# Kernel tuning notes

Hardware: AMD Instinct MI355X
Metric: run time of the kernel (lower is better)

## Reference

```python
import jax, jax.numpy as jnp
import numpy as np

B, L, F = 8, 2048, 4
DM, DI, N, DCONV, DTRANK = 320, 1280, 16, 8, 20  # d_model, d_inner, d_state, d_conv, dt_rank
NBLK = 4


def setup_inputs() -> dict:
    key = jax.random.key(0)
    ks = jax.random.split(key, 24)
    s = 0.05
    inp = {
        "x": jax.random.uniform(ks[0], (B, L, F), jnp.float32),
        "fc_w": jax.random.normal(ks[1], (320, 4), jnp.float32) * s,
        "fc_b": jnp.zeros((320,), jnp.float32),
        "blk_lin_w": jax.random.normal(ks[2], (NBLK, 320, 320), jnp.float32) * s,
        "blk_lin_b": jnp.zeros((NBLK, 320), jnp.float32),
        "blk_inproj_w": jax.random.normal(ks[3], (NBLK, 2 * DI, DM), jnp.float32) * s,
        "blk_conv_w": jax.random.normal(ks[4], (NBLK, DI, DCONV), jnp.float32) * s,
        "blk_conv_b": jnp.zeros((NBLK, DI), jnp.float32),
        "blk_xproj_w": jax.random.normal(ks[5], (NBLK, DTRANK + 2 * N, DI), jnp.float32) * s,
        "blk_dtproj_w": jax.random.normal(ks[6], (NBLK, DI, DTRANK), jnp.float32) * s,
        "blk_dtproj_b": jnp.full((NBLK, DI), -4.0, jnp.float32),  # softplus(-4) ~ 0.018, stable dt
        "blk_A_log": jnp.tile(jnp.log(jnp.arange(1, N + 1, dtype=jnp.float32)), (NBLK, DI, 1)),
        "blk_D": jnp.ones((NBLK, DI), jnp.float32),
        "blk_outproj_w": jax.random.normal(ks[7], (NBLK, DM, DI), jnp.float32) * s,
        "s1_w1": jax.random.normal(ks[8], (512, 320), jnp.float32) * s,
        "s1_b1": jnp.zeros((512,), jnp.float32),
        "s1_w2": jax.random.normal(ks[9], (512, 512), jnp.float32) * s,
        "s1_b2": jnp.zeros((512,), jnp.float32),
        "s1_w3": jax.random.normal(ks[10], (1, 512), jnp.float32) * s,
        "s1_b3": jnp.zeros((1,), jnp.float32),
    }
    return inp


def _mamba(u, inproj_w, conv_w, conv_b, xproj_w, dtproj_w, dtproj_b, A_log, D):
    # u: (B, L, DM)
    xz = u @ inproj_w.T                       # (B, L, 2*DI)
    x, z = jnp.split(xz, 2, axis=-1)
    # causal depthwise conv1d over time
    xc = jnp.transpose(x, (0, 2, 1))          # (B, DI, L)
    xc = jax.lax.conv_general_dilated(
        xc, conv_w[:, None, :], (1,), [(DCONV - 1, 0)],
        feature_group_count=DI, dimension_numbers=("NCH", "OIH", "NCH"))
    xc = xc + conv_b[None, :, None]
    x = jax.nn.silu(jnp.transpose(xc, (0, 2, 1)))  # (B, L, DI)
    dbc = x @ xproj_w.T                        # (B, L, DTRANK + 2N)
    dt, Bm, Cm = jnp.split(dbc, [DTRANK, DTRANK + N], axis=-1)
    delta = jax.nn.softplus(dt @ dtproj_w.T + dtproj_b)  # (B, L, DI)
    A = -jnp.exp(A_log)                        # (DI, N)

    def step(h, inp):
        xt, dt_t, Bt, Ct = inp                 # (B,DI),(B,DI),(B,N),(B,N)
        dA = jnp.exp(dt_t[..., None] * A)      # (B, DI, N)
        h = dA * h + (dt_t * xt)[..., None] * Bt[:, None, :]
        y = jnp.einsum("bdn,bn->bd", h, Ct)
        return h, y

    h0 = jnp.zeros((u.shape[0], DI, N), x.dtype)
    xs = (jnp.swapaxes(x, 0, 1), jnp.swapaxes(delta, 0, 1),
          jnp.swapaxes(Bm, 0, 1), jnp.swapaxes(Cm, 0, 1))
    _, ys = jax.lax.scan(step, h0, xs)         # ys: (L, B, DI)
    y = jnp.swapaxes(ys, 0, 1) + x * D         # (B, L, DI)
    y = y * jax.nn.silu(z)
    return y


def reference(x, fc_w, fc_b, blk_lin_w, blk_lin_b, blk_inproj_w, blk_conv_w,
              blk_conv_b, blk_xproj_w, blk_dtproj_w, blk_dtproj_b, blk_A_log,
              blk_D, blk_outproj_w, s1_w1, s1_b1, s1_w2, s1_b2, s1_w3, s1_b3):
    seq_len = x.shape[1]
    start_max = jnp.max(x[:, :, 2])
    xn = jnp.stack([x[:, :, 0] / 255.0,
                    x[:, :, 1] / 255.0,
                    x[:, :, 2] / start_max,
                    x[:, :, 3]], axis=-1)
    out = xn @ fc_w.T + fc_b                   # (B, L, 320)
    for i in range(NBLK):
        out = jnp.tanh(out @ blk_lin_w[i].T + blk_lin_b[i])
        out = _mamba(out, blk_inproj_w[i], blk_conv_w[i], blk_conv_b[i],
                     blk_xproj_w[i], blk_dtproj_w[i], blk_dtproj_b[i],
                     blk_A_log[i], blk_D[i]) @ blk_outproj_w[i].T
        out = jax.nn.elu(out)                  # dropout p=1e-6 -> identity (eval)
    h = out[:, -1, :]                          # (B, 320)
    h = jax.nn.relu(h @ s1_w1.T + s1_b1)
    h = jax.nn.relu(h @ s1_w2.T + s1_b2)
    h = h @ s1_w3.T + s1_b3                    # (B, 1)
    scale = start_max / (1.0 + np.log(seq_len))
    h = h.at[:, 0].multiply(scale)
    return jax.nn.relu(h)
```

## Files before the change

kernel.cpp:

```cpp
#include <hip/hip_runtime.h>
#include <math.h>

#define BSZ 8
#define LSZ 2048
#define DMV 320
#define DIV 1280
#define NST 16
#define DCV 8
#define DTR 20
#define NBLKV 4
#define MTOT (BSZ*LSZ)
#define NCHUNK 32
#define CLEN 64
#define DBLD 56

typedef __attribute__((ext_vector_type(8))) short short8;
typedef __attribute__((ext_vector_type(8))) unsigned short ushort8;
typedef __attribute__((ext_vector_type(4))) float floatx4;

__device__ inline unsigned short f2bf(float f) {
    union { float f; unsigned u; } v; v.f = f;
    unsigned r = v.u + 0x7FFFu + ((v.u >> 16) & 1u);
    return (unsigned short)(r >> 16);
}
__device__ inline float bf2f(unsigned short b) {
    union { unsigned u; float f; } v; v.u = ((unsigned)b) << 16;
    return v.f;
}

__device__ __forceinline__ void gload_lds16(unsigned short* l, const unsigned short* g) {
    __builtin_amdgcn_global_load_lds(
        (const __attribute__((address_space(1))) unsigned int*)g,
        (__attribute__((address_space(3))) unsigned int*)l, 16, 0, 0);
}

__global__ __launch_bounds__(256) void convert_kernel(
    const float* __restrict__ src, unsigned short* __restrict__ dst, long n4) {
    long i = (long)blockIdx.x * 256 + threadIdx.x;
    if (i >= n4) return;
    float4 v = *(const float4*)(src + i * 4);
    unsigned short o[4] = {f2bf(v.x), f2bf(v.y), f2bf(v.z), f2bf(v.w)};
    *(unsigned long long*)(dst + i * 4) = *(unsigned long long*)o;
}

__global__ __launch_bounds__(256) void convert_dtw_kernel(
    const float* __restrict__ src, unsigned short* __restrict__ dst) {
    int i = blockIdx.x * 256 + threadIdx.x;
    if (i >= NBLKV * DIV * 32) return;
    int l = i / (DIV * 32), rem = i % (DIV * 32);
    int d = rem >> 5, j = rem & 31;
    dst[i] = (j < DTR) ? f2bf(src[((long)l * DIV + d) * DTR + j]) : (unsigned short)0;
}

__global__ __launch_bounds__(256) void convert_xp_kernel(
    const float* __restrict__ src, unsigned short* __restrict__ dst) {
    int i = blockIdx.x * 256 + threadIdx.x;
    if (i >= NBLKV * 64 * DIV) return;
    int l = i / (64 * DIV), rem = i % (64 * DIV);
    int n = rem / DIV, k = rem % DIV;
    dst[i] = (n < DTR + 2 * NST) ? f2bf(src[((long)l * (DTR + 2 * NST) + n) * DIV + k])
                                 : (unsigned short)0;
}

__global__ __launch_bounds__(256) void convert_t2_kernel(
    const float* __restrict__ src, unsigned short* __restrict__ dst, int N, int K) {
    int i = blockIdx.x * 256 + threadIdx.x;
    if (i >= N * K) return;
    int n = i / K, k = i % K;
    dst[((k >> 1) * N + n) * 2 + (k & 1)] = f2bf(src[i]);
}

__global__ void init_sm_kernel(float* sm) {
    if (threadIdx.x == 0) ((int*)sm)[0] = 0;
}

__global__ void reduce_max_kernel(const float* __restrict__ x, float* sm) {
    int idx = blockIdx.x * blockDim.x + threadIdx.x;
    float v = 0.f;
    for (int i = idx; i < MTOT; i += gridDim.x * blockDim.x)
        v = fmaxf(v, x[i * 4 + 2]);
    #pragma unroll
    for (int off = 32; off > 0; off >>= 1)
        v = fmaxf(v, __shfl_xor(v, off, 64));
    if ((threadIdx.x & 63) == 0)
        atomicMax((int*)sm, __float_as_int(v));
}

__global__ __launch_bounds__(256) void fc_kernel(
    const float* __restrict__ x, const float* __restrict__ fw,
    const float* __restrict__ fb, const float* __restrict__ sm,
    unsigned short* __restrict__ u) {
    int o = blockIdx.x * 64 + (threadIdx.x & 63);
    long m = (long)blockIdx.y * 4 + (threadIdx.x >> 6);
    float inv_sm = 1.0f / sm[0];
    float x0 = x[m * 4 + 0] * (1.0f / 255.0f);
    float x1 = x[m * 4 + 1] * (1.0f / 255.0f);
    float x2 = x[m * 4 + 2] * inv_sm;
    float x3 = x[m * 4 + 3];
    float acc = fb[o];
    acc = fmaf(x0, fw[o * 4 + 0], acc);
    acc = fmaf(x1, fw[o * 4 + 1], acc);
    acc = fmaf(x2, fw[o * 4 + 2], acc);
    acc = fmaf(x3, fw[o * 4 + 3], acc);
    u[m * DMV + o] = f2bf(acc);
}

template<int ACT, int BM, int BN, int KB, typename TOUT>
__global__ __launch_bounds__(256) void gemm_mfma_kernel(
    const unsigned short* __restrict__ X, const unsigned short* __restrict__ W,
    const float* __restrict__ bias, TOUT* __restrict__ Y,
    int N, int K, long ldx, long ldy)
{
    constexpr int WMT = (BM == 128 && BN == 128) ? 4 : 2;
    constexpr int WNT = (BM == 64 && BN == 64) ? 2 : 4;
    constexpr int CPR = KB / 8;
    constexpr int CMSK = CPR - 1;
    constexpr int NCX = BM * CPR / 256;
    constexpr int NCW = BN * CPR / 256;
    __shared__ unsigned short Xs[BM * KB];
    __shared__ unsigned short Ws[BN * KB];

    int tid = threadIdx.x;
    int wave = tid >> 6, lane = tid & 63;
    int quad = lane >> 4, l15 = lane & 15;
    int wmbase, wnbase;
    if (BM == 128 && BN == 128)      { wmbase = (wave & 1) * 64; wnbase = (wave >> 1) * 64; }
    else if (BM == 128 && BN == 64)  { wmbase = wave * 32;       wnbase = 0; }
    else                             { wmbase = (wave & 1) * 32; wnbase = (wave >> 1) * 32; }
    long m0 = (long)blockIdx.y * BM;
    int n0 = blockIdx.x * BN;

    floatx4 acc[WMT][WNT];
    #pragma unroll
    for (int i = 0; i < WMT; i++)
        #pragma unroll
        for (int j = 0; j < WNT; j++)
            acc[i][j] = (floatx4){0.f, 0.f, 0.f, 0.f};

    const unsigned short* Xb = X + m0 * ldx;
    const unsigned short* Wb = W + (long)n0 * K;

    for (int k0 = 0; k0 < K; k0 += KB) {
        #pragma unroll
        for (int j = 0; j < NCX; j++) {
            int s = (wave * NCX + j) * 64 + lane;
            int r = s / CPR, c = s % CPR;
            int cg = c ^ (r & CMSK);
            gload_lds16(&Xs[(wave * NCX + j) * 512],
                        Xb + (long)r * ldx + k0 + cg * 8);
        }
        #pragma unroll
        for (int j = 0; j < NCW; j++) {
            int s = (wave * NCW + j) * 64 + lane;
            int r = s / CPR, c = s % CPR;
            int cg = c ^ (r & CMSK);
            gload_lds16(&Ws[(wave * NCW + j) * 512],
                        Wb + (long)r * K + k0 + cg * 8);
        }
        __syncthreads();
        #pragma unroll
        for (int kk = 0; kk < KB; kk += 32) {
            short8 af[WMT], bfr[WNT];
            #pragma unroll
            for (int i = 0; i < WMT; i++) {
                int R = wmbase + i * 16 + l15;
                int cp = (kk / 8 + quad) ^ (R & CMSK);
                af[i] = *(short8*)&Xs[R * KB + cp * 8];
            }
            #pragma unroll
            for (int j = 0; j < WNT; j++) {
                int R = wnbase + j * 16 + l15;
                int cp = (kk / 8 + quad) ^ (R & CMSK);
                bfr[j] = *(short8*)&Ws[R * KB + cp * 8];
            }
            #pragma unroll
            for (int i = 0; i < WMT; i++)
                #pragma unroll
                for (int j = 0; j < WNT; j++)
                    acc[i][j] = __builtin_amdgcn_mfma_f32_16x16x32_bf16(
                        af[i], bfr[j], acc[i][j], 0, 0, 0);
        }
        __syncthreads();
    }

    #pragma unroll
    for (int i = 0; i < WMT; i++) {
        long mb = m0 + wmbase + i * 16 + quad * 4;
        #pragma unroll
        for (int j = 0; j < WNT; j++) {
            int n = n0 + wnbase + j * 16 + l15;
            if (n >= N) continue;
            float bv = bias ? bias[n] : 0.f;
            #pragma unroll
            for (int r = 0; r < 4; r++) {
                float v = acc[i][j][r] + bv;
                if (ACT == 1) v = tanhf(v);
                else if (ACT == 3) v = (v > 0.f) ? v : expm1f(v);
                else if (ACT == 4) v = (v > 20.f) ? v : __logf(1.0f + __expf(v));
                if constexpr (sizeof(TOUT) == 2)
                    Y[(mb + r) * ldy + n] = f2bf(v);
                else
                    Y[(mb + r) * ldy + n] = v;
            }
        }
    }
}

__global__ __launch_bounds__(512) void head_kernel(
    const unsigned short* __restrict__ u,
    const unsigned short* __restrict__ w1t, const float* __restrict__ b1,
    const unsigned short* __restrict__ w2t, const float* __restrict__ b2,
    const float* __restrict__ w3, const float* __restrict__ b3,
    const float* __restrict__ sm, float* __restrict__ out)
{
    __shared__ float xs[DMV];
    __shared__ float h1s[512];
    __shared__ float red[8];
    int b = blockIdx.x;
    int tid = threadIdx.x;
    const unsigned short* xr = u + ((long)b * LSZ + (LSZ - 1)) * DMV;
    if (tid < DMV) xs[tid] = bf2f(xr[tid]);
    __syncthreads();

    float acc = 0.f;
    #pragma unroll 8
    for (int kk = 0; kk < DMV / 2; kk++) {
        unsigned wv = *(const unsigned*)&w1t[((long)kk * 512 + tid) * 2];
        acc = fmaf(xs[2 * kk],     bf2f((unsigned short)(wv & 0xffffu)), acc);
        acc = fmaf(xs[2 * kk + 1], bf2f((unsigned short)(wv >> 16)), acc);
    }
    h1s[tid] = fmaxf(acc + b1[tid], 0.f);
    __syncthreads();

    acc = 0.f;
    #pragma unroll 8
    for (int kk = 0; kk < 256; kk++) {
        unsigned wv = *(const unsigned*)&w2t[((long)kk * 512 + tid) * 2];
        acc = fmaf(h1s[2 * kk],     bf2f((unsigned short)(wv & 0xffffu)), acc);
        acc = fmaf(h1s[2 * kk + 1], bf2f((unsigned short)(wv >> 16)), acc);
    }
    float h2 = fmaxf(acc + b2[tid], 0.f);

    float part = h2 * w3[tid];
    #pragma unroll
    for (int off = 32; off > 0; off >>= 1) part += __shfl_xor(part, off, 64);
    if ((tid & 63) == 0) red[tid >> 6] = part;
    __syncthreads();
    if (tid == 0) {
        float s = b3[0];
        #pragma unroll
        for (int w = 0; w < 8; w++) s += red[w];
        float scale = sm[0] / 8.624618986159398f;
        out[b] = fmaxf(s * scale, 0.f);
    }
}

#define TCONV 32
__global__ __launch_bounds__(256) void conv_kernel(
    const unsigned short* __restrict__ xz, const float* __restrict__ cw,
    const float* __restrict__ cb, unsigned short* __restrict__ xc)
{
    int d = blockIdx.x * 256 + threadIdx.x;
    int lb = blockIdx.z;
    int l0 = blockIdx.y * TCONV;
    long base = (long)lb * LSZ + l0;

    float w[8];
    #pragma unroll
    for (int k = 0; k < 8; k++) w[k] = cw[d * 8 + k];
    float bc = cb[d];

    float win[8];
    #pragma unroll
    for (int i = 0; i < 7; i++) {
        int l = l0 - 7 + i;
        win[i] = (l >= 0) ? bf2f(xz[(base - 7 + i) * 2560 + d]) : 0.f;
    }
    #pragma unroll
    for (int s = 0; s < TCONV; s++) {
        win[7] = bf2f(xz[(base + s) * 2560 + d]);
        float acc = bc;
        #pragma unroll
        for (int k = 0; k < 8; k++) acc = fmaf(win[k], w[k], acc);
        float sv = acc / (1.0f + __expf(-acc));
        xc[(base + s) * DIV + d] = f2bf(sv);
        #pragma unroll
        for (int k = 0; k < 7; k++) win[k] = win[k + 1];
    }
}

__device__ inline void pow_ladder(float p, float* pw) {
    pw[0] = p;
    pw[1] = pw[0] * pw[0];
    pw[2] = pw[1] * pw[0];
    pw[3] = pw[1] * pw[1];
    pw[4] = pw[3] * pw[0];
    pw[5] = pw[3] * pw[1];
    pw[6] = pw[3] * pw[2];
    pw[7] = pw[3] * pw[3];
    #pragma unroll
    for (int k = 8; k < 16; k++) pw[k] = pw[7] * pw[k - 8];
}

__global__ __launch_bounds__(256) void scan_local_kernel(
    const unsigned short* __restrict__ xc, unsigned short* xz,
    const unsigned short* __restrict__ dbc, unsigned short* delta,
    const float* __restrict__ A_log, const float* __restrict__ Dp,
    float* __restrict__ hfin, float* __restrict__ sumd)
{
    __shared__ float S[CLEN * 32];
    int lb = blockIdx.z;
    int ch = blockIdx.y;
    int d = blockIdx.x * 256 + threadIdx.x;
    int tid = threadIdx.x;

    float a[NST], h[NST];
    #pragma unroll
    for (int n = 0; n < NST; n++) {
        a[n] = -__expf(A_log[d * NST + n]);
        h[n] = 0.f;
    }
    float a0 = a[0];
    bool geo = true;
    #pragma unroll
    for (int n = 1; n < NST; n++)
        geo = geo && (fabsf(a[n] - (float)(n + 1) * a0) <= 1e-4f * (float)(n + 1));
    float Dd = Dp[d];

    long tok0 = (long)lb * LSZ + ch * CLEN;
    for (int i = tid; i < CLEN * 32; i += 256) {
        int r = i >> 5, c = i & 31;
        S[i] = bf2f(dbc[(tok0 + r) * DBLD + 20 + c]);
    }
    __syncthreads();

    float sd = 0.f;
    if (__all(geo)) {
        for (int l = 0; l < CLEN; l++) {
            long m = tok0 + l;
            const float* row = &S[l * 32];
            float dl = bf2f(delta[m * DIV + d]);
            sd += dl;
            delta[m * DIV + d] = f2bf(sd);
            float xv = bf2f(xc[m * DIV + d]);
            float db = dl * xv;
            float pw[NST];
            pow_ladder(__expf(dl * a0), pw);
            float y = 0.f;
            #pragma unroll
            for (int n = 0; n < NST; n++) {
                h[n] = fmaf(pw[n], h[n], db * row[n]);
                y = fmaf(h[n], row[16 + n], y);
            }
            y = fmaf(xv, Dd, y);
            xz[m * 2560 + d] = f2bf(y);
        }
    } else {
        for (int l = 0; l < CLEN; l++) {
            long m = tok0 + l;
            const float* row = &S[l * 32];
            float dl = bf2f(delta[m * DIV + d]);
            sd += dl;
            delta[m * DIV + d] = f2bf(sd);
            float xv = bf2f(xc[m * DIV + d]);
            float db = dl * xv;
            float y = 0.f;
            #pragma unroll
            for (int n = 0; n < NST; n++) {
                float dA = __expf(dl * a[n]);
                h[n] = fmaf(dA, h[n], db * row[n]);
                y = fmaf(h[n], row[16 + n], y);
            }
            y = fmaf(xv, Dd, y);
            xz[m * 2560 + d] = f2bf(y);
        }
    }

    long cidx = ((long)lb * NCHUNK + ch) * DIV + d;
    #pragma unroll
    for (int n = 0; n < NST; n++) hfin[cidx * NST + n] = h[n];
    sumd[cidx] = sd;
}

__global__ __launch_bounds__(256) void scan_prefix_kernel(
    float* __restrict__ hfin, const float* __restrict__ sumd,
    const float* __restrict__ A_log, int Bc)
{
    long g = (long)blockIdx.x * 256 + threadIdx.x;
    int n = (int)(g & (NST - 1));
    long t = g >> 4;
    int d = (int)(t % DIV);
    int lb = (int)(t / DIV);
    if (lb >= Bc) return;

    float a = -__expf(A_log[d * NST + n]);
    float s = 0.f;
    for (int c = 0; c < NCHUNK; c++) {
        long cidx = ((long)lb * NCHUNK + c) * DIV + d;
        float hl = hfin[cidx * NST + n];
        float P = __expf(a * sumd[cidx]);
        hfin[cidx * NST + n] = s;
        s = fmaf(P, s, hl);
    }
}

__global__ __launch_bounds__(256) void scan_fix_kernel(
    unsigned short* xz, const unsigned short* __restrict__ dbc,
    const unsigned short* __restrict__ cum,
    const float* __restrict__ A_log, const float* __restrict__ hfin)
{
    __shared__ float S[CLEN * 16];
    int lb = blockIdx.z;
    int ch = blockIdx.y;
    int d = blockIdx.x * 256 + threadIdx.x;
    int tid = threadIdx.x;

    float a[NST], hin[NST];
    #pragma unroll
    for (int n = 0; n < NST; n++) a[n] = -__expf(A_log[d * NST + n]);
    float a0 = a[0];
    bool geo = true;
    #pragma unroll
    for (int n = 1; n < NST; n++)
        geo = geo && (fabsf(a[n] - (float)(n + 1) * a0) <= 1e-4f * (float)(n + 1));

    long cidx = ((long)lb * NCHUNK + ch) * DIV + d;
    #pragma unroll
    for (int n = 0; n < NST; n += 4)
        *(float4*)&hin[n] = *(const float4*)&hfin[cidx * NST + n];

    long tok0 = (long)lb * LSZ + ch * CLEN;
    for (int i = tid; i < CLEN * 16; i += 256) {
        int r = i >> 4, c = i & 15;
        S[i] = bf2f(dbc[(tok0 + r) * DBLD + 36 + c]);
    }
    __syncthreads();

    if (__all(geo)) {
        for (int l = 0; l < CLEN; l++) {
            long m = tok0 + l;
            const float* row = &S[l * 16];
            float cm = bf2f(cum[m * DIV + d]);
            float pw[NST];
            pow_ladder(__expf(cm * a0), pw);
            float fix = 0.f;
            #pragma unroll
            for (int n = 0; n < NST; n++)
                fix = fmaf(hin[n] * pw[n], row[n], fix);
            float y = bf2f(xz[m * 2560 + d]) + fix;
            float zv = bf2f(xz[m * 2560 + 1280 + d]);
            float sz = zv / (1.0f + __expf(-zv));
            xz[m * 2560 + d] = f2bf(y * sz);
        }
    } else {
        for (int l = 0; l < CLEN; l++) {
            long m = tok0 + l;
            const float* row = &S[l * 16];
            float cm = bf2f(cum[m * DIV + d]);
            float fix = 0.f;
            #pragma unroll
            for (int n = 0; n < NST; n++)
                fix = fmaf(hin[n] * __expf(cm * a[n]), row[n], fix);
            float y = bf2f(xz[m * 2560 + d]) + fix;
            float zv = bf2f(xz[m * 2560 + 1280 + d]);
            float sz = zv / (1.0f + __expf(-zv));
            xz[m * 2560 + d] = f2bf(y * sz);
        }
    }
}

extern "C" void kernel_launch(void* const* d_in, const int* in_sizes, int n_in,
                              void* d_out, int out_size, void* d_ws, size_t ws_size,
                              hipStream_t stream) {
    const float* x        = (const float*)d_in[0];
    const float* fc_w     = (const float*)d_in[1];
    const float* fc_b     = (const float*)d_in[2];
    const float* lin_w    = (const float*)d_in[3];
    const float* lin_b    = (const float*)d_in[4];
    const float* inproj_w = (const float*)d_in[5];
    const float* conv_w   = (const float*)d_in[6];
    const float* conv_b   = (const float*)d_in[7];
    const float* xproj_w  = (const float*)d_in[8];
    const float* dtproj_w = (const float*)d_in[9];
    const float* dtproj_b = (const float*)d_in[10];
    const float* A_log    = (const float*)d_in[11];
    const float* Dp       = (const float*)d_in[12];
    const float* outproj_w= (const float*)d_in[13];
    const float* s1_w1    = (const float*)d_in[14];
    const float* s1_b1    = (const float*)d_in[15];
    const float* s1_w2    = (const float*)d_in[16];
    const float* s1_b2    = (const float*)d_in[17];
    const float* s1_w3    = (const float*)d_in[18];
    const float* s1_b3    = (const float*)d_in[19];

    const long NLIN = (long)NBLKV * DMV * DMV;
    const long NINP = (long)NBLKV * 2 * DIV * DMV;
    const long NXPP = (long)NBLKV * 64 * DIV;
    const long NOUT = (long)NBLKV * DMV * DIV;
    const long NDTW = (long)NBLKV * DIV * 32;
    const long NHW1 = (long)512 * DMV;
    const long NHW2 = (long)512 * 512;

    const long FIXED = 256 +
                       (NLIN + NINP + NXPP + NOUT + NDTW + NHW1 + NHW2) * 2 + 256;
    const long PER_BATCH = (long)LSZ * (DMV + DMV + 2 * DIV + DIV) * 2
                         + (long)LSZ * DBLD * 2
                         + (long)LSZ * DIV * 2
                         + (long)NCHUNK * DIV * NST * 4
                         + (long)NCHUNK * DIV * 4;
    int Bc = 8;
    while (Bc > 1 && (size_t)(FIXED + (long)Bc * PER_BATCH) > ws_size)
        Bc >>= 1;
    int nchunk_b = BSZ / Bc;
    long Mc = (long)Bc * LSZ;

    char* p = (char*)d_ws;
    float* sm = (float*)p;           p += 256;
    unsigned short* wlin = (unsigned short*)p; p += NLIN * 2;
    unsigned short* winp = (unsigned short*)p; p += NINP * 2;
    unsigned short* wxp  = (unsigned short*)p; p += NXPP * 2;
    unsigned short* wout = (unsigned short*)p; p += NOUT * 2;
    unsigned short* wdt  = (unsigned short*)p; p += NDTW * 2;
    unsigned short* w1t  = (unsigned short*)p; p += NHW1 * 2;
    unsigned short* w2t  = (unsigned short*)p; p += NHW2 * 2;
    unsigned short* u  = (unsigned short*)p;   p += Mc * DMV * 2;
    unsigned short* t  = (unsigned short*)p;   p += Mc * DMV * 2;
    unsigned short* xz = (unsigned short*)p;   p += Mc * 2560 * 2;
    unsigned short* xc = (unsigned short*)p;   p += Mc * DIV * 2;
    unsigned short* dbc = (unsigned short*)p;  p += Mc * DBLD * 2;
    unsigned short* delta = (unsigned short*)p; p += Mc * DIV * 2;
    float* hfin = (float*)p;         p += (long)Bc * NCHUNK * DIV * NST * 4;
    float* sumd = (float*)p;

    convert_kernel<<<(unsigned)((NLIN / 4 + 255) / 256), 256, 0, stream>>>(lin_w, wlin, NLIN / 4);
    convert_kernel<<<(unsigned)((NINP / 4 + 255) / 256), 256, 0, stream>>>(inproj_w, winp, NINP / 4);
    convert_kernel<<<(unsigned)((NOUT / 4 + 255) / 256), 256, 0, stream>>>(outproj_w, wout, NOUT / 4);
    convert_xp_kernel<<<(unsigned)((NXPP + 255) / 256), 256, 0, stream>>>(xproj_w, wxp);
    convert_dtw_kernel<<<(unsigned)((NDTW + 255) / 256), 256, 0, stream>>>(dtproj_w, wdt);
    convert_t2_kernel<<<(unsigned)((NHW1 + 255) / 256), 256, 0, stream>>>(s1_w1, w1t, 512, DMV);
    convert_t2_kernel<<<(unsigned)((NHW2 + 255) / 256), 256, 0, stream>>>(s1_w2, w2t, 512, 512);

    init_sm_kernel<<<1, 64, 0, stream>>>(sm);
    reduce_max_kernel<<<32, 256, 0, stream>>>(x, sm);

    for (int c = 0; c < nchunk_b; c++) {
        int b0 = c * Bc;
        fc_kernel<<<dim3(5, (unsigned)(Mc / 4)), 256, 0, stream>>>(
            x + (long)b0 * LSZ * 4, fc_w, fc_b, sm, u);

        for (int i = 0; i < NBLKV; i++) {
            const float* lb  = lin_b    + (long)i * DMV;
            const float* cw  = conv_w   + (long)i * DIV * DCV;
            const float* cb  = conv_b   + (long)i * DIV;
            const float* dpb = dtproj_b + (long)i * DIV;
            const float* al  = A_log    + (long)i * DIV * NST;
            const float* dd  = Dp       + (long)i * DIV;

            gemm_mfma_kernel<1, 128, 64, 64, unsigned short>
                <<<dim3(5, (unsigned)(Mc / 128)), 256, 0, stream>>>(
                u, wlin + (long)i * DMV * DMV, lb, t, DMV, DMV, DMV, DMV);
            gemm_mfma_kernel<0, 128, 128, 64, unsigned short>
                <<<dim3(20, (unsigned)(Mc / 128)), 256, 0, stream>>>(
                t, winp + (long)i * 2 * DIV * DMV, nullptr, xz, 2 * DIV, DMV, DMV, 2 * DIV);
            conv_kernel<<<dim3(5, LSZ / TCONV, Bc), 256, 0, stream>>>(xz, cw, cb, xc);
            gemm_mfma_kernel<0, 64, 64, 64, unsigned short>
                <<<dim3(1, (unsigned)(Mc / 64)), 256, 0, stream>>>(
                xc, wxp + (long)i * 64 * DIV, nullptr, dbc,
                DTR + 2 * NST, DIV, DIV, DBLD);
            gemm_mfma_kernel<4, 128, 128, 32, unsigned short>
                <<<dim3(10, (unsigned)(Mc / 128)), 256, 0, stream>>>(
                dbc, wdt + (long)i * DIV * 32, dpb, delta, DIV, 32, DBLD, DIV);
            scan_local_kernel<<<dim3(5, NCHUNK, Bc), 256, 0, stream>>>(
                xc, xz, dbc, delta, al, dd, hfin, sumd);
            scan_prefix_kernel<<<dim3(Bc * 80), 256, 0, stream>>>(hfin, sumd, al, Bc);
            scan_fix_kernel<<<dim3(5, NCHUNK, Bc), 256, 0, stream>>>(
                xz, dbc, delta, al, hfin);
            gemm_mfma_kernel<3, 128, 64, 64, unsigned short>
                <<<dim3(5, (unsigned)(Mc / 128)), 256, 0, stream>>>(
                xz, wout + (long)i * DMV * DIV, nullptr, u, DMV, DIV, 2 * DIV, DMV);
        }

        head_kernel<<<Bc, 512, 0, stream>>>(u, w1t, s1_b1, w2t, s1_b2,
                                            s1_w3, s1_b3, sm, (float*)d_out + b0);
    }
}
```

Before: 1.275 ms.

## Halve scan chunk length, store chunk states in bf16, recompute cumulative delta

Chunk length drops from 64 to 32 and the chunk count doubles from 32 to 64, which gives the chunked selective scan more parallel blocks and shorter serial loops. The local scan no longer writes the running delta sum back to memory; the fix-up kernel rebuilds it by accumulating delta itself. Per-chunk carried states are stored in bf16 instead of fp32 to cut their traffic. The cost is a longer serial prefix loop over more chunks and some extra precision loss in the carried states.

```diff
diff --git a/kernel.cpp b/kernel.cpp
--- a/kernel.cpp
+++ b/kernel.cpp
@@ -10,8 +10,8 @@
 #define DTR 20
 #define NBLKV 4
 #define MTOT (BSZ*LSZ)
-#define NCHUNK 32
-#define CLEN 64
+#define NCHUNK 64
+#define CLEN 32
 #define DBLD 56
 
 typedef __attribute__((ext_vector_type(8))) short short8;
@@ -304,9 +304,9 @@
 
 __global__ __launch_bounds__(256) void scan_local_kernel(
     const unsigned short* __restrict__ xc, unsigned short* xz,
-    const unsigned short* __restrict__ dbc, unsigned short* delta,
+    const unsigned short* __restrict__ dbc, const unsigned short* __restrict__ delta,
     const float* __restrict__ A_log, const float* __restrict__ Dp,
-    float* __restrict__ hfin, float* __restrict__ sumd)
+    unsigned short* __restrict__ hfin, float* __restrict__ sumd)
 {
     __shared__ float S[CLEN * 32];
     int lb = blockIdx.z;
@@ -341,7 +341,6 @@
             const float* row = &S[l * 32];
             float dl = bf2f(delta[m * DIV + d]);
             sd += dl;
-            delta[m * DIV + d] = f2bf(sd);
             float xv = bf2f(xc[m * DIV + d]);
             float db = dl * xv;
             float pw[NST];
@@ -361,7 +360,6 @@
             const float* row = &S[l * 32];
             float dl = bf2f(delta[m * DIV + d]);
             sd += dl;
-            delta[m * DIV + d] = f2bf(sd);
             float xv = bf2f(xc[m * DIV + d]);
             float db = dl * xv;
             float y = 0.f;
@@ -378,12 +376,12 @@
 
     long cidx = ((long)lb * NCHUNK + ch) * DIV + d;
     #pragma unroll
-    for (int n = 0; n < NST; n++) hfin[cidx * NST + n] = h[n];
+    for (int n = 0; n < NST; n++) hfin[cidx * NST + n] = f2bf(h[n]);
     sumd[cidx] = sd;
 }
 
 __global__ __launch_bounds__(256) void scan_prefix_kernel(
-    float* __restrict__ hfin, const float* __restrict__ sumd,
+    unsigned short* __restrict__ hfin, const float* __restrict__ sumd,
     const float* __restrict__ A_log, int Bc)
 {
     long g = (long)blockIdx.x * 256 + threadIdx.x;
@@ -397,17 +395,17 @@
     float s = 0.f;
     for (int c = 0; c < NCHUNK; c++) {
         long cidx = ((long)lb * NCHUNK + c) * DIV + d;
-        float hl = hfin[cidx * NST + n];
+        float hl = bf2f(hfin[cidx * NST + n]);
         float P = __expf(a * sumd[cidx]);
-        hfin[cidx * NST + n] = s;
+        hfin[cidx * NST + n] = f2bf(s);
         s = fmaf(P, s, hl);
     }
 }
 
 __global__ __launch_bounds__(256) void scan_fix_kernel(
     unsigned short* xz, const unsigned short* __restrict__ dbc,
-    const unsigned short* __restrict__ cum,
-    const float* __restrict__ A_log, const float* __restrict__ hfin)
+    const unsigned short* __restrict__ delta,
+    const float* __restrict__ A_log, const unsigned short* __restrict__ hfin)
 {
     __shared__ float S[CLEN * 16];
     int lb = blockIdx.z;
@@ -426,8 +424,7 @@
 
     long cidx = ((long)lb * NCHUNK + ch) * DIV + d;
     #pragma unroll
-    for (int n = 0; n < NST; n += 4)
-        *(float4*)&hin[n] = *(const float4*)&hfin[cidx * NST + n];
+    for (int n = 0; n < NST; n++) hin[n] = bf2f(hfin[cidx * NST + n]);
 
     long tok0 = (long)lb * LSZ + ch * CLEN;
     for (int i = tid; i < CLEN * 16; i += 256) {
@@ -436,13 +433,14 @@
     }
     __syncthreads();
 
+    float cum = 0.f;
     if (__all(geo)) {
         for (int l = 0; l < CLEN; l++) {
             long m = tok0 + l;
             const float* row = &S[l * 16];
-            float cm = bf2f(cum[m * DIV + d]);
+            cum += bf2f(delta[m * DIV + d]);
             float pw[NST];
-            pow_ladder(__expf(cm * a0), pw);
+            pow_ladder(__expf(cum * a0), pw);
             float fix = 0.f;
             #pragma unroll
             for (int n = 0; n < NST; n++)
@@ -456,11 +454,11 @@
         for (int l = 0; l < CLEN; l++) {
             long m = tok0 + l;
             const float* row = &S[l * 16];
-            float cm = bf2f(cum[m * DIV + d]);
+            cum += bf2f(delta[m * DIV + d]);
             float fix = 0.f;
             #pragma unroll
             for (int n = 0; n < NST; n++)
-                fix = fmaf(hin[n] * __expf(cm * a[n]), row[n], fix);
+                fix = fmaf(hin[n] * __expf(cum * a[n]), row[n], fix);
             float y = bf2f(xz[m * 2560 + d]) + fix;
             float zv = bf2f(xz[m * 2560 + 1280 + d]);
             float sz = zv / (1.0f + __expf(-zv));
@@ -506,7 +504,7 @@
     const long PER_BATCH = (long)LSZ * (DMV + DMV + 2 * DIV + DIV) * 2
                          + (long)LSZ * DBLD * 2
                          + (long)LSZ * DIV * 2
-                         + (long)NCHUNK * DIV * NST * 4
+                         + (long)NCHUNK * DIV * NST * 2
                          + (long)NCHUNK * DIV * 4;
     int Bc = 8;
     while (Bc > 1 && (size_t)(FIXED + (long)Bc * PER_BATCH) > ws_size)
@@ -529,7 +527,7 @@
     unsigned short* xc = (unsigned short*)p;   p += Mc * DIV * 2;
     unsigned short* dbc = (unsigned short*)p;  p += Mc * DBLD * 2;
     unsigned short* delta = (unsigned short*)p; p += Mc * DIV * 2;
-    float* hfin = (float*)p;         p += (long)Bc * NCHUNK * DIV * NST * 4;
+    unsigned short* hfin = (unsigned short*)p; p += (long)Bc * NCHUNK * DIV * NST * 2;
     float* sumd = (float*)p;
 
     convert_kernel<<<(unsigned)((NLIN / 4 + 255) / 256), 256, 0, stream>>>(lin_w, wlin, NLIN / 4);
```

After: 1.234 ms. 1.03x faster.
